# Kernel tuning notes

Hardware: AMD Instinct MI355X
Metric: run time of the kernel (lower is better)

## Reference

```python
import jax, jax.numpy as jnp
import numpy as np

IGNORE_INDEX = -100


def setup_inputs() -> dict:
    key = jax.random.key(0)
    k1, k2, k3 = jax.random.split(key, 3)
    N, H, V = 4096, 2048, 50257
    x = jax.random.normal(k1, (N, H), dtype=jnp.float32)
    weight = jax.random.normal(k2, (V, H), dtype=jnp.float32) * (1.0 / np.sqrt(H))
    y = jax.random.randint(k3, (N,), 0, V, dtype=jnp.int64)
    return {"x": x, "weight": weight, "y": y}


def reference(x, weight, y):
    # Fused linear + cross entropy: logits = x @ W^T, mean NLL over non-ignored tokens.
    logits = jnp.einsum("nh,vh->nv", x, weight)  # [N, V]
    logp = jax.nn.log_softmax(logits, axis=-1)
    mask = (y != IGNORE_INDEX)
    safe_y = jnp.where(mask, y, 0)
    nll = -jnp.take_along_axis(logp, safe_y[:, None], axis=-1)[:, 0]  # [N]
    n_valid = jnp.maximum(jnp.sum(mask), 1)
    loss = jnp.sum(jnp.where(mask, nll, 0.0)) / n_valid.astype(nll.dtype)
    return loss
```

## Files before the change

kernel.cpp:

```cpp
#include <hip/hip_runtime.h>
#include <hip/hip_bf16.h>
#include <math.h>

typedef unsigned char  u8;
typedef unsigned int   u32;
typedef __attribute__((ext_vector_type(8)))  int   int8v;
typedef __attribute__((ext_vector_type(16))) float f32x16;

typedef __attribute__((address_space(3))) void lds_void;
typedef __attribute__((address_space(1))) void gbl_void;

#define IGNORE_INDEX (-100)

__device__ __forceinline__ u8 f32_to_e4m3(float f) {
    union { float f; u32 u; } v; v.f = f;
    u32 s  = (v.u >> 24) & 0x80u;
    u32 au = v.u & 0x7FFFFFFFu;
    float a = __uint_as_float(au);
    if (a >= 448.0f) return (u8)(s | 0x7E);
    int e = (int)(au >> 23) - 127;
    if (e >= -6) {
        u32 m    = au & 0x7FFFFFu;
        u32 keep = m >> 20;
        u32 rest = m & 0xFFFFFu;
        keep += (rest > 0x80000u) || (rest == 0x80000u && (keep & 1u));
        u32 code = ((u32)(e + 7) << 3) + keep;
        if (code > 0x7E) code = 0x7E;
        return (u8)(s | code);
    } else {
        int q = (int)rintf(a * 512.0f);
        return (u8)(s | (u32)q);
    }
}

__global__ __launch_bounds__(256) void cvt_f32_fp8(const float* __restrict__ in,
                                                   u8* __restrict__ out,
                                                   float scale, long n) {
    long i = (long)blockIdx.x * blockDim.x + threadIdx.x;
    long stride = (long)gridDim.x * blockDim.x;
    for (long j = i * 16; j + 15 < n; j += stride * 16) {
        u8 tmp[16];
#pragma unroll
        for (int t = 0; t < 4; ++t) {
            float4 f = *(const float4*)(in + j + t * 4);
            tmp[t * 4 + 0] = f32_to_e4m3(f.x * scale);
            tmp[t * 4 + 1] = f32_to_e4m3(f.y * scale);
            tmp[t * 4 + 2] = f32_to_e4m3(f.z * scale);
            tmp[t * 4 + 3] = f32_to_e4m3(f.w * scale);
        }
        *(int4*)(out + j) = *(const int4*)tmp;
    }
}

__global__ __launch_bounds__(256) void gemm_lse_partial(
    const u8* __restrict__ A8,
    const u8* __restrict__ B8,
    float2* __restrict__ partials,
    int H, int V, int VT)
{
    constexpr int BM = 128, BKB = 128;
    __shared__ __align__(16) u8 As[BM * BKB];
    __shared__ __align__(16) u8 Bs[BM * BKB];

    const int tid  = threadIdx.x;
    const int w    = tid >> 6;
    const int lane = tid & 63;
    const int wm   = w >> 1, wn = w & 1;
    const int half = lane >> 5;
    const int ln32 = lane & 31;

    const int mBase = blockIdx.x * BM;
    const int vTile = blockIdx.y;
    const int vBase = vTile * BM;

    const int rsub = lane >> 3;
    const int csub = lane & 7;
    const int sch  = csub ^ rsub;

    int aRow[4], bRow[4];
#pragma unroll
    for (int c = 0; c < 4; ++c) {
        int band = w * 4 + c;
        int r = band * 8 + rsub;
        aRow[c] = mBase + r;
        int vr = vBase + r;
        bRow[c] = (vr < V) ? vr : (V - 1);
    }

    f32x16 acc[2][2];
#pragma unroll
    for (int i = 0; i < 2; ++i)
#pragma unroll
        for (int j = 0; j < 2; ++j)
#pragma unroll
            for (int r = 0; r < 16; ++r) acc[i][j][r] = 0.0f;

    const int scaleA = 0x7C7C7C7C;
    const int scaleB = 0x7B7B7B7B;

    const size_t Hs = (size_t)H;
    for (int k0 = 0; k0 < H; k0 += BKB) {
#pragma unroll
        for (int c = 0; c < 4; ++c) {
            int band = w * 4 + c;
            const u8* gA = A8 + (size_t)aRow[c] * Hs + k0 + sch * 16;
            const u8* gB = B8 + (size_t)bRow[c] * Hs + k0 + sch * 16;
            __builtin_amdgcn_global_load_lds((gbl_void*)gA, (lds_void*)(As + band * 1024), 16, 0, 0);
            __builtin_amdgcn_global_load_lds((gbl_void*)gB, (lds_void*)(Bs + band * 1024), 16, 0, 0);
        }
        __syncthreads();

#pragma unroll
        for (int ks = 0; ks < 2; ++ks) {
            int8v af[2], bf[2];
            const int c0 = ks * 4 + half * 2;
#pragma unroll
            for (int i = 0; i < 2; ++i) {
                int ar = wm * 64 + i * 32 + ln32;
                int sw = ar & 7;
                int4 lo = *(const int4*)(As + ar * 128 + ((c0    ) ^ sw) * 16);
                int4 hi = *(const int4*)(As + ar * 128 + ((c0 + 1) ^ sw) * 16);
                int8v a; a[0]=lo.x; a[1]=lo.y; a[2]=lo.z; a[3]=lo.w;
                         a[4]=hi.x; a[5]=hi.y; a[6]=hi.z; a[7]=hi.w;
                af[i] = a;
                int br = wn * 64 + i * 32 + ln32;
                sw = br & 7;
                lo = *(const int4*)(Bs + br * 128 + ((c0    ) ^ sw) * 16);
                hi = *(const int4*)(Bs + br * 128 + ((c0 + 1) ^ sw) * 16);
                int8v b; b[0]=lo.x; b[1]=lo.y; b[2]=lo.z; b[3]=lo.w;
                         b[4]=hi.x; b[5]=hi.y; b[6]=hi.z; b[7]=hi.w;
                bf[i] = b;
            }
#pragma unroll
            for (int i = 0; i < 2; ++i)
#pragma unroll
                for (int j = 0; j < 2; ++j)
                    acc[i][j] = __builtin_amdgcn_mfma_scale_f32_32x32x64_f8f6f4(
                        af[i], bf[j], acc[i][j], 0, 0, 0, scaleA, 0, scaleB);
        }
        __syncthreads();
    }

    bool vj[2];
#pragma unroll
    for (int j = 0; j < 2; ++j)
        vj[j] = (vBase + wn * 64 + j * 32 + ln32) < V;

    float2* red = (float2*)As;

#pragma unroll
    for (int i = 0; i < 2; ++i) {
#pragma unroll
        for (int r = 0; r < 16; ++r) {
            float v0 = vj[0] ? acc[i][0][r] : -INFINITY;
            float v1 = vj[1] ? acc[i][1][r] : -INFINITY;
            float m = fmaxf(v0, v1);
#pragma unroll
            for (int o = 1; o < 32; o <<= 1)
                m = fmaxf(m, __shfl_xor(m, o, 64));
            float s = 0.0f;
            if (vj[0]) s += __expf(acc[i][0][r] - m);
            if (vj[1]) s += __expf(acc[i][1][r] - m);
#pragma unroll
            for (int o = 1; o < 32; o <<= 1)
                s += __shfl_xor(s, o, 64);
            if (ln32 == 0) {
                int row = wm * 64 + i * 32 + (r & 3) + 8 * (r >> 2) + 4 * half;
                red[row * 2 + wn] = make_float2(m, s);
            }
        }
    }
    __syncthreads();

    if (tid < BM) {
        float2 p0 = red[tid * 2 + 0];
        float2 p1 = red[tid * 2 + 1];
        float m = fmaxf(p0.x, p1.x);
        float s = p0.y * __expf(p0.x - m) + p1.y * __expf(p1.x - m);
        partials[(size_t)(mBase + tid) * VT + vTile] = make_float2(m, s);
    }
}

__global__ __launch_bounds__(256) void row_final(
    const float* __restrict__ x,
    const float* __restrict__ W,
    const int* __restrict__ y,
    const float2* __restrict__ partials,
    float* __restrict__ nll, float* __restrict__ valid,
    int H, int V, int VT)
{
    const int n = blockIdx.x;
    const int t = threadIdx.x;
    const int yn = y[n];
    const bool ok = (yn != IGNORE_INDEX);

    float dsum = 0.0f;
    if (ok) {
        int cy = yn; if (cy < 0) cy = 0; if (cy >= V) cy = V - 1;
        const float4* xr = (const float4*)(x + (size_t)n * H);
        const float4* wr = (const float4*)(W + (size_t)cy * H);
        int nf4 = H >> 2;
        for (int i = t; i < nf4; i += 256) {
            float4 a = xr[i], b = wr[i];
            dsum += a.x * b.x + a.y * b.y + a.z * b.z + a.w * b.w;
        }
    }

    float m = -INFINITY, s = 0.0f;
    const float2* pr = partials + (size_t)n * VT;
    for (int i = t; i < VT; i += 256) {
        float2 p = pr[i];
        float nm = fmaxf(m, p.x);
        s = s * __expf(m - nm) + p.y * __expf(p.x - nm);
        m = nm;
    }

    __shared__ float rm[256], rs[256], rd[256];
    rm[t] = m; rs[t] = s; rd[t] = dsum;
    __syncthreads();
    for (int o = 128; o > 0; o >>= 1) {
        if (t < o) {
            float m2 = rm[t + o], s2 = rs[t + o];
            float nm = fmaxf(rm[t], m2);
            rs[t] = rs[t] * __expf(rm[t] - nm) + s2 * __expf(m2 - nm);
            rm[t] = nm;
            rd[t] += rd[t + o];
        }
        __syncthreads();
    }
    if (t == 0) {
        float lse = rm[0] + __logf(rs[0]);
        nll[n]   = ok ? (lse - rd[0]) : 0.0f;
        valid[n] = ok ? 1.0f : 0.0f;
    }
}

__global__ __launch_bounds__(1024) void final_loss(
    const float* __restrict__ nll, const float* __restrict__ valid,
    float* __restrict__ out, int n)
{
    __shared__ float ss[1024], sv[1024];
    const int t = threadIdx.x;
    float a = 0.0f, b = 0.0f;
    for (int i = t; i < n; i += 1024) { a += nll[i]; b += valid[i]; }
    ss[t] = a; sv[t] = b;
    __syncthreads();
    for (int o = 512; o > 0; o >>= 1) {
        if (t < o) { ss[t] += ss[t + o]; sv[t] += sv[t + o]; }
        __syncthreads();
    }
    if (t == 0) out[0] = ss[0] / fmaxf(sv[0], 1.0f);
}

extern "C" void kernel_launch(void* const* d_in, const int* in_sizes, int n_in,
                              void* d_out, int out_size, void* d_ws, size_t ws_size,
                              hipStream_t stream) {
    const float* x = (const float*)d_in[0];
    const float* W = (const float*)d_in[1];
    const int*   y = (const int*)d_in[2];

    const long xsz = in_sizes[0];
    const long wsz = in_sizes[1];
    const int  N   = in_sizes[2];
    const int  H   = (int)(xsz / N);
    const int  V   = (int)(wsz / H);
    const int  VT  = (V + 127) / 128;
    const int  MT  = N / 128;

    char* ws = (char*)d_ws;
    size_t off = 0;
    u8* Wf8 = (u8*)(ws + off); off += (size_t)wsz; off = (off + 255) & ~(size_t)255;
    u8* Xf8 = (u8*)(ws + off); off += (size_t)xsz; off = (off + 255) & ~(size_t)255;
    float2* partials = (float2*)(ws + off); off += (size_t)N * VT * sizeof(float2); off = (off + 255) & ~(size_t)255;
    float* nll   = (float*)(ws + off); off += (size_t)N * 4;
    float* valid = (float*)(ws + off); off += (size_t)N * 4;

    int wBlocks = (int)((wsz / 16 + 255) / 256);
    int xBlocks = (int)((xsz / 16 + 255) / 256);
    cvt_f32_fp8<<<wBlocks, 256, 0, stream>>>(W, Wf8, 16.0f, wsz);
    cvt_f32_fp8<<<xBlocks, 256, 0, stream>>>(x, Xf8, 8.0f, xsz);

    dim3 grid(MT, VT);
    gemm_lse_partial<<<grid, 256, 0, stream>>>(Xf8, Wf8, partials, H, V, VT);

    row_final<<<N, 256, 0, stream>>>(x, W, y, partials, nll, valid, H, V, VT);
    final_loss<<<1, 1024, 0, stream>>>(nll, valid, (float*)d_out, N);
}
```

Baseline: 1.210 ms.

## Store LDS tiles in MFMA fragment order for conflict-free contiguous reads

```diff
diff --git a/kernel.cpp b/kernel.cpp
--- a/kernel.cpp
+++ b/kernel.cpp
@@ -58,34 +58,26 @@
     float2* __restrict__ partials,
     int H, int V, int VT)
 {
-    constexpr int BM = 128, BKB = 128;
-    __shared__ __align__(16) u8 As[BM * BKB];
-    __shared__ __align__(16) u8 Bs[BM * BKB];
+    __shared__ __align__(16) u8 As[16 * 1024];
+    __shared__ __align__(16) u8 Bs[16 * 1024];
 
     const int tid  = threadIdx.x;
     const int w    = tid >> 6;
     const int lane = tid & 63;
     const int wm   = w >> 1, wn = w & 1;
-    const int half = lane >> 5;
     const int ln32 = lane & 31;
-
-    const int mBase = blockIdx.x * BM;
+    const int khalf = lane >> 5;
+
+    const int mBase = blockIdx.x * 128;
     const int vTile = blockIdx.y;
-    const int vBase = vTile * BM;
-
-    const int rsub = lane >> 3;
-    const int csub = lane & 7;
-    const int sch  = csub ^ rsub;
-
-    int aRow[4], bRow[4];
-#pragma unroll
-    for (int c = 0; c < 4; ++c) {
-        int band = w * 4 + c;
-        int r = band * 8 + rsub;
-        aRow[c] = mBase + r;
-        int vr = vBase + r;
-        bRow[c] = (vr < V) ? vr : (V - 1);
-    }
+    const int vBase = vTile * 128;
+
+    const size_t Hs = (size_t)H;
+    const size_t aRow = (size_t)(mBase + w * 32 + ln32);
+    int vr = vBase + w * 32 + ln32; if (vr >= V) vr = V - 1;
+    const u8* aBase = A8 + aRow * Hs + khalf * 32;
+    const u8* bBase = B8 + (size_t)vr * Hs + khalf * 32;
+    const int cOff0 = 0, cOff1 = 16, cOff2 = 64, cOff3 = 80;
 
     f32x16 acc[2][2];
 #pragma unroll
@@ -98,35 +90,36 @@
     const int scaleA = 0x7C7C7C7C;
     const int scaleB = 0x7B7B7B7B;
 
-    const size_t Hs = (size_t)H;
-    for (int k0 = 0; k0 < H; k0 += BKB) {
-#pragma unroll
-        for (int c = 0; c < 4; ++c) {
-            int band = w * 4 + c;
-            const u8* gA = A8 + (size_t)aRow[c] * Hs + k0 + sch * 16;
-            const u8* gB = B8 + (size_t)bRow[c] * Hs + k0 + sch * 16;
-            __builtin_amdgcn_global_load_lds((gbl_void*)gA, (lds_void*)(As + band * 1024), 16, 0, 0);
-            __builtin_amdgcn_global_load_lds((gbl_void*)gB, (lds_void*)(Bs + band * 1024), 16, 0, 0);
-        }
+    const u8* aRd = As + lane * 16;
+    const u8* bRd = Bs + lane * 16;
+
+    for (int k0 = 0; k0 < H; k0 += 128) {
+        u8* aDst = (u8*)As + w * 4096;
+        u8* bDst = (u8*)Bs + w * 4096;
+        __builtin_amdgcn_global_load_lds((gbl_void*)(aBase + k0 + cOff0), (lds_void*)(aDst       ), 16, 0, 0);
+        __builtin_amdgcn_global_load_lds((gbl_void*)(aBase + k0 + cOff1), (lds_void*)(aDst + 1024), 16, 0, 0);
+        __builtin_amdgcn_global_load_lds((gbl_void*)(aBase + k0 + cOff2), (lds_void*)(aDst + 2048), 16, 0, 0);
+        __builtin_amdgcn_global_load_lds((gbl_void*)(aBase + k0 + cOff3), (lds_void*)(aDst + 3072), 16, 0, 0);
+        __builtin_amdgcn_global_load_lds((gbl_void*)(bBase + k0 + cOff0), (lds_void*)(bDst       ), 16, 0, 0);
+        __builtin_amdgcn_global_load_lds((gbl_void*)(bBase + k0 + cOff1), (lds_void*)(bDst + 1024), 16, 0, 0);
+        __builtin_amdgcn_global_load_lds((gbl_void*)(bBase + k0 + cOff2), (lds_void*)(bDst + 2048), 16, 0, 0);
+        __builtin_amdgcn_global_load_lds((gbl_void*)(bBase + k0 + cOff3), (lds_void*)(bDst + 3072), 16, 0, 0);
         __syncthreads();
 
 #pragma unroll
         for (int ks = 0; ks < 2; ++ks) {
             int8v af[2], bf[2];
-            const int c0 = ks * 4 + half * 2;
 #pragma unroll
             for (int i = 0; i < 2; ++i) {
-                int ar = wm * 64 + i * 32 + ln32;
-                int sw = ar & 7;
-                int4 lo = *(const int4*)(As + ar * 128 + ((c0    ) ^ sw) * 16);
-                int4 hi = *(const int4*)(As + ar * 128 + ((c0 + 1) ^ sw) * 16);
+                int sA = ((wm * 2 + i) * 4 + ks * 2) * 1024;
+                int4 lo = *(const int4*)(aRd + sA);
+                int4 hi = *(const int4*)(aRd + sA + 1024);
                 int8v a; a[0]=lo.x; a[1]=lo.y; a[2]=lo.z; a[3]=lo.w;
                          a[4]=hi.x; a[5]=hi.y; a[6]=hi.z; a[7]=hi.w;
                 af[i] = a;
-                int br = wn * 64 + i * 32 + ln32;
-                sw = br & 7;
-                lo = *(const int4*)(Bs + br * 128 + ((c0    ) ^ sw) * 16);
-                hi = *(const int4*)(Bs + br * 128 + ((c0 + 1) ^ sw) * 16);
+                int sB = ((wn * 2 + i) * 4 + ks * 2) * 1024;
+                lo = *(const int4*)(bRd + sB);
+                hi = *(const int4*)(bRd + sB + 1024);
                 int8v b; b[0]=lo.x; b[1]=lo.y; b[2]=lo.z; b[3]=lo.w;
                          b[4]=hi.x; b[5]=hi.y; b[6]=hi.z; b[7]=hi.w;
                 bf[i] = b;
@@ -165,14 +158,14 @@
             for (int o = 1; o < 32; o <<= 1)
                 s += __shfl_xor(s, o, 64);
             if (ln32 == 0) {
-                int row = wm * 64 + i * 32 + (r & 3) + 8 * (r >> 2) + 4 * half;
+                int row = wm * 64 + i * 32 + (r & 3) + 8 * (r >> 2) + 4 * khalf;
                 red[row * 2 + wn] = make_float2(m, s);
             }
         }
     }
     __syncthreads();
 
-    if (tid < BM) {
+    if (tid < 128) {
         float2 p0 = red[tid * 2 + 0];
         float2 p1 = red[tid * 2 + 1];
         float m = fmaxf(p0.x, p1.x);
```

Result: slower. 1.350 ms (+11.5%).
